# Kernel optimization log

Measured on AMD Instinct MI355X. Metric: run time of the kernel, lower is better.

Reference implementation:

```python
import jax, jax.numpy as jnp
import numpy as np

B, R, H, IN, L = 8, 128, 256, 512, 3
NH, DH = 4, H // 4  # attention heads


def _layernorm(x, g, b, eps=1e-5):
    mu = jnp.mean(x, axis=-1, keepdims=True)
    var = jnp.mean(jnp.square(x - mu), axis=-1, keepdims=True)
    return (x - mu) * jax.lax.rsqrt(var + eps) * g + b


def setup_inputs() -> dict:
    key = jax.random.key(0)
    ks = iter(jax.random.split(key, 40))
    s = 0.02
    d = {}
    d['x'] = jax.random.normal(next(ks), (B, IN), jnp.float32)
    d['We'] = jax.random.normal(next(ks), (IN, H), jnp.float32) * s
    d['be'] = jnp.zeros((H,), jnp.float32)
    # per-graph-layer params, stacked along leading L axis
    d['msg_W1'] = jax.random.normal(next(ks), (L, 2 * H, H), jnp.float32) * s
    d['msg_b1'] = jnp.zeros((L, H), jnp.float32)
    d['msg_W2'] = jax.random.normal(next(ks), (L, H, H), jnp.float32) * s
    d['msg_b2'] = jnp.zeros((L, H), jnp.float32)
    d['upd_W1'] = jax.random.normal(next(ks), (L, 2 * H, H), jnp.float32) * s
    d['upd_b1'] = jnp.zeros((L, H), jnp.float32)
    d['upd_W2'] = jax.random.normal(next(ks), (L, H, H), jnp.float32) * s
    d['upd_b2'] = jnp.zeros((L, H), jnp.float32)
    d['ln_g'] = jnp.ones((L, H), jnp.float32)
    d['ln_b'] = jnp.zeros((L, H), jnp.float32)
    d['rule_adj'] = jax.random.normal(next(ks), (R, R), jnp.float32)
    # multihead attention (4 heads)
    d['Wq'] = jax.random.normal(next(ks), (H, H), jnp.float32) * s
    d['bq'] = jnp.zeros((H,), jnp.float32)
    d['Wk'] = jax.random.normal(next(ks), (H, H), jnp.float32) * s
    d['bk'] = jnp.zeros((H,), jnp.float32)
    d['Wv'] = jax.random.normal(next(ks), (H, H), jnp.float32) * s
    d['bv'] = jnp.zeros((H,), jnp.float32)
    d['Wo'] = jax.random.normal(next(ks), (H, H), jnp.float32) * s
    d['bo'] = jnp.zeros((H,), jnp.float32)
    # readout MLP -> num_rules logits
    d['ro_W1'] = jax.random.normal(next(ks), (H, H), jnp.float32) * s
    d['ro_b1'] = jnp.zeros((H,), jnp.float32)
    d['ro_W2'] = jax.random.normal(next(ks), (H, R), jnp.float32) * s
    d['ro_b2'] = jnp.zeros((R,), jnp.float32)
    return d


def reference(x, We, be, msg_W1, msg_b1, msg_W2, msg_b2,
              upd_W1, upd_b1, upd_W2, upd_b2, ln_g, ln_b, rule_adj,
              Wq, bq, Wk, bk, Wv, bv, Wo, bo,
              ro_W1, ro_b1, ro_W2, ro_b2):
    # node encoder, broadcast to all rule-graph nodes: [B,R,H]
    h0 = x @ We + be
    h = jnp.broadcast_to(h0[:, None, :], (B, R, H))
    # rule adjacency with self-edges excluded (loop used i != j)
    A = jax.nn.sigmoid(rule_adj) * (1.0 - jnp.eye(R, dtype=rule_adj.dtype))  # [R,R]
    for l in range(L):
        # message_net(cat(h_i, h_j)) = relu(h_i@W1a + h_j@W1b + b1)@W2 + b2
        W1a, W1b = msg_W1[l][:H], msg_W1[l][H:]
        a = h @ W1a   # [B,R,H] (receiver i part)
        bb = h @ W1b  # [B,R,H] (sender j part)
        pre = jax.nn.relu(a[:, :, None, :] + bb[:, None, :, :] + msg_b1[l])  # [B,R,R,H]
        m = pre @ msg_W2[l] + msg_b2[l]  # [B,R,R,H] message from j to i
        agg = jnp.einsum('bijh,ij->bih', m, A)  # weighted sum over senders j
        # update_net(cat(h, agg))
        Wu1a, Wu1b = upd_W1[l][:H], upd_W1[l][H:]
        u = jax.nn.relu(h @ Wu1a + agg @ Wu1b + upd_b1[l]) @ upd_W2[l] + upd_b2[l]
        h = _layernorm(h + u, ln_g[l], ln_b[l])
    # multihead self-attention over nodes
    q = (h @ Wq + bq).reshape(B, R, NH, DH)
    k = (h @ Wk + bk).reshape(B, R, NH, DH)
    v = (h @ Wv + bv).reshape(B, R, NH, DH)
    logits = jnp.einsum('bqhd,bkhd->bhqk', q, k) / jnp.sqrt(jnp.float32(DH))
    attn = jax.nn.softmax(logits, axis=-1)
    pooled = jnp.einsum('bhqk,bkhd->bqhd', attn, v).reshape(B, R, H) @ Wo + bo
    g = jnp.mean(pooled, axis=1)  # [B,H]
    rule_logits = jax.nn.relu(g @ ro_W1 + ro_b1) @ ro_W2 + ro_b2
    rule_probabilities = jax.nn.softmax(rule_logits, axis=-1)  # [B,R]
    return rule_probabilities
```

## Files before the change

### kernel.cpp

```cpp
#include <hip/hip_runtime.h>
#include <math.h>

constexpr int NB  = 8;
constexpr int NR  = 128;
constexpr int HID = 256;
constexpr int NIN = 512;
constexpr int DHD = 64;
constexpr size_t SZ = (size_t)NB * NR * HID;

struct KP {
    const float *x, *We, *be, *msg_W1, *msg_b1, *msg_W2, *msg_b2;
    const float *upd_W1, *upd_b1, *upd_W2, *upd_b2, *ln_g, *ln_b, *rule_adj;
    const float *Wq, *bq, *Wk, *bk, *Wv, *bv, *Wo, *bo, *ro_W1, *ro_b1, *ro_W2, *ro_b2;
    float* out;
    float *N0, *N1, *N2;
    float *aB, *bbB, *p1B;
    float *aA, *bbA, *p1A;
    float *W2u, *mb2u, *Aw, *rsum;
    float *mW1s;
    float *h0g, *c0g, *c1g;
    float *gacc;
    float *scratch;
};

__device__ __forceinline__ void gemm_core(
    float (&As)[16][68], float (&Bs)[16][64], int m0, int n0,
    const float* __restrict__ A, const float* __restrict__ B,
    float (&acc)[4][4])
{
    int tid = threadIdx.x;
    int ty = tid >> 4, tx = tid & 15;
    int arow = tid >> 2, acol = (tid & 3) << 2;
    int brow = tid >> 4, bcol = (tid & 15) << 2;
    int m = m0 + arow;

    float4 av = *(const float4*)&A[(size_t)m * HID + acol];
    float4 bv = *(const float4*)&B[(size_t)brow * HID + n0 + bcol];

    for (int k0 = 0; k0 < HID; k0 += 16) {
        As[acol + 0][arow] = av.x;
        As[acol + 1][arow] = av.y;
        As[acol + 2][arow] = av.z;
        As[acol + 3][arow] = av.w;
        *(float4*)&Bs[brow][bcol] = bv;
        __syncthreads();
        if (k0 + 16 < HID) {
            av = *(const float4*)&A[(size_t)m * HID + k0 + 16 + acol];
            bv = *(const float4*)&B[(size_t)(k0 + 16 + brow) * HID + n0 + bcol];
        }
#pragma unroll
        for (int kk = 0; kk < 16; ++kk) {
            float4 af = *(const float4*)&As[kk][ty << 2];
            float4 bf = *(const float4*)&Bs[kk][tx << 2];
            float a_[4] = {af.x, af.y, af.z, af.w};
            float b_[4] = {bf.x, bf.y, bf.z, bf.w};
#pragma unroll
            for (int i = 0; i < 4; ++i)
#pragma unroll
                for (int j = 0; j < 4; ++j) acc[i][j] += a_[i] * b_[j];
        }
        __syncthreads();
    }
}

__device__ __forceinline__ void gemv256w(
    const float* xs, const float* __restrict__ W,
    const float* __restrict__ bias, int relu, float* ys, float* red)
{
    int tid = threadIdx.x;
    int w = tid >> 6, l = tid & 63;
    float4 acc = {0.f, 0.f, 0.f, 0.f};
    const float* Wp = W + (size_t)(w * 64) * HID + l * 4;
    const float* xp = xs + w * 64;
#pragma unroll 16
    for (int kk = 0; kk < 64; ++kk) {
        float xv = xp[kk];
        float4 wv = *(const float4*)(Wp + (size_t)kk * HID);
        acc.x += xv * wv.x; acc.y += xv * wv.y;
        acc.z += xv * wv.z; acc.w += xv * wv.w;
    }
    *(float4*)&red[w * 256 + l * 4] = acc;
    __syncthreads();
    float v = red[tid] + red[256 + tid] + red[512 + tid] + red[768 + tid];
    if (bias) v += bias[tid];
    if (relu) v = fmaxf(v, 0.0f);
    ys[tid] = v;
    __syncthreads();
}

__device__ __forceinline__ void rows4_half(
    const float (&rows)[4][HID], const float* __restrict__ W,
    int col, int half, float o[4])
{
    o[0] = o[1] = o[2] = o[3] = 0.f;
    int kbase = half * 128;
#pragma unroll 4
    for (int k0 = 0; k0 < 128; k0 += 4) {
        int k = kbase + k0;
        float w0 = W[(size_t)(k + 0) * HID + col];
        float w1 = W[(size_t)(k + 1) * HID + col];
        float w2 = W[(size_t)(k + 2) * HID + col];
        float w3 = W[(size_t)(k + 3) * HID + col];
#pragma unroll
        for (int ii = 0; ii < 4; ++ii) {
            float4 rv = *(const float4*)&rows[ii][k];
            o[ii] += rv.x * w0 + rv.y * w1 + rv.z * w2 + rv.w * w3;
        }
    }
}

__device__ __forceinline__ void ln_stats4_512(
    float (&sred)[4][4][2], float (&mi)[4][2], const float v[4], int half)
{
    if (half == 0) {
        int w = threadIdx.x >> 6, l = threadIdx.x & 63;
        float s[4], q[4];
#pragma unroll
        for (int ii = 0; ii < 4; ++ii) { s[ii] = v[ii]; q[ii] = v[ii] * v[ii]; }
#pragma unroll
        for (int off = 32; off; off >>= 1) {
#pragma unroll
            for (int ii = 0; ii < 4; ++ii) {
                s[ii] += __shfl_xor(s[ii], off);
                q[ii] += __shfl_xor(q[ii], off);
            }
        }
        if (l == 0) {
#pragma unroll
            for (int ii = 0; ii < 4; ++ii) { sred[w][ii][0] = s[ii]; sred[w][ii][1] = q[ii]; }
        }
    }
    __syncthreads();
    if (threadIdx.x < 4) {
        int r = threadIdx.x;
        float ss = sred[0][r][0] + sred[1][r][0] + sred[2][r][0] + sred[3][r][0];
        float qq = sred[0][r][1] + sred[1][r][1] + sred[2][r][1] + sred[3][r][1];
        float mu = ss * (1.0f / HID);
        mi[r][0] = mu;
        mi[r][1] = rsqrtf(qq * (1.0f / HID) - mu * mu + 1e-5f);
    }
    __syncthreads();
}

__global__ __launch_bounds__(256) void setup0_kernel(KP P) {
    __shared__ union {
        struct { float As[16][68]; float Bs[16][64]; } g;
        struct { float xs[NIN]; float part[8][32]; } e;
    } L;
    int blk = blockIdx.x;
    int t = threadIdx.x;

    if (blk < 32) {
        int rr = blk * 4 + (t >> 6);
        int l = t & 63;
        float s_loc = 0.f;
#pragma unroll
        for (int rep = 0; rep < 2; ++rep) {
            int j = l + rep * 64;
            float xv = P.rule_adj[rr * NR + j];
            float sg = 1.0f / (1.0f + expf(-xv));
            if (j == rr) sg = 0.0f;
            P.Aw[rr * NR + j] = sg;
            s_loc += sg;
        }
#pragma unroll
        for (int off = 32; off; off >>= 1) s_loc += __shfl_xor(s_loc, off);
        if (l == 0) P.rsum[rr] = s_loc;
    } else if (blk < 80) {
        int idx = blk - 32, l2 = idx >> 4, t16 = idx & 15;
        int m0 = (t16 >> 2) * 64, n0 = (t16 & 3) * 64;
        float acc[4][4] = {};
        gemm_core(L.g.As, L.g.Bs, m0, n0,
                  P.msg_W2 + (size_t)l2 * HID * HID,
                  P.upd_W1 + (size_t)l2 * 2 * HID * HID + (size_t)HID * HID,
                  acc);
        int ty = t >> 4, tx = t & 15;
        float* C = P.W2u + (size_t)l2 * HID * HID;
#pragma unroll
        for (int i = 0; i < 4; ++i) {
            int m = m0 + (ty << 2) + i, n = n0 + (tx << 2);
            float4 o = {acc[i][0], acc[i][1], acc[i][2], acc[i][3]};
            *(float4*)&C[(size_t)m * HID + n] = o;
        }
    } else if (blk < 83) {
        int l2 = blk - 80;
        const float* b2v = P.msg_b2 + l2 * HID;
        const float* Bm = P.upd_W1 + (size_t)l2 * 2 * HID * HID + (size_t)HID * HID;
        float acc = 0.f;
#pragma unroll 4
        for (int k = 0; k < HID; ++k) acc += b2v[k] * Bm[(size_t)k * HID + t];
        P.mb2u[l2 * HID + t] = acc;
    } else if (blk < 147) {
        int idx = blk - 83;
        int b = idx >> 3, s = idx & 7;
        L.e.xs[t]       = P.x[b * NIN + t];
        L.e.xs[256 + t] = P.x[b * NIN + 256 + t];
        __syncthreads();
        int c = t & 31, seg = t >> 5;
        int col = s * 32 + c;
        const float* Wp = P.We + (size_t)(seg * 64) * HID + col;
        const float* xp = L.e.xs + seg * 64;
        float acc = 0.f;
#pragma unroll 16
        for (int k = 0; k < 64; ++k) acc += xp[k] * Wp[(size_t)k * HID];
        L.e.part[seg][c] = acc;
        __syncthreads();
        if (t < 32) {
            float v = 0.f;
#pragma unroll
            for (int sg = 0; sg < 8; ++sg) v += L.e.part[sg][t];
            int cc = s * 32 + t;
            P.h0g[b * HID + cc] = v + P.be[cc];
        }
    } else if (blk < 163) {
        int base = (blk - 147) * 4096;
        for (int i = t; i < 4096; i += 256) {
            int o = base + i;
            P.mW1s[o] = P.msg_W1[o] + P.msg_W1[65536 + o];
        }
    } else {
        int pfid = blk - 163, npf = 256 - 163;
        const float* arr[11] = {P.We, P.msg_W1, P.msg_W2, P.upd_W1, P.upd_W2,
                                P.Wq, P.Wk, P.Wv, P.Wo, P.ro_W1, P.ro_W2};
        const int n4[11] = {32768, 98304, 49152, 98304, 49152,
                            16384, 16384, 16384, 16384, 16384, 8192};
        float s = 0.f;
        for (int a = 0; a < 11; ++a) {
            const float4* p4 = (const float4*)arr[a];
            for (int i = pfid * 256 + t; i < n4[a]; i += npf * 256) {
                float4 v = p4[i];
                s += v.x + v.y + v.z + v.w;
            }
        }
        if (s == 1.0e37f) P.scratch[pfid] = s;
    }
}

__global__ __launch_bounds__(256) void headc_kernel(KP P) {
    __shared__ float h0s[HID];
    __shared__ float p0s[HID];
    __shared__ float part[8][32];
    int blk = blockIdx.x;
    int z = blk >> 6, bs = blk & 63;
    int b = bs >> 3, s = bs & 7;
    int t = threadIdx.x;
    h0s[t] = P.h0g[b * HID + t];
    __syncthreads();
    const float* Wslice;
    const float* xs;
    if (z == 0) {
        Wslice = P.upd_W1;
        xs = h0s;
    } else {
        float accp = 0.f;
#pragma unroll 8
        for (int k = 0; k < HID; ++k)
            accp += h0s[k] * P.mW1s[(size_t)k * HID + t];
        p0s[t] = fmaxf(accp + P.msg_b1[t], 0.0f);
        __syncthreads();
        Wslice = P.W2u;
        xs = p0s;
    }
    int c = t & 31, seg = t >> 5;
    int col = s * 32 + c;
    const float* Wp = Wslice + (size_t)(seg * 32) * HID + col;
    const float* xp = xs + seg * 32;
    float acc = 0.f;
#pragma unroll 8
    for (int k = 0; k < 32; ++k) acc += xp[k] * Wp[(size_t)k * HID];
    part[seg][c] = acc;
    __syncthreads();
    if (t < 32) {
        float v = 0.f;
#pragma unroll
        for (int sg = 0; sg < 8; ++sg) v += part[sg][t];
        int cc = s * 32 + t;
        if (z == 0) P.c0g[b * HID + cc] = v;
        else        P.c1g[b * HID + cc] = v + P.mb2u[cc];
    }
}

__global__ __launch_bounds__(512) void layer0p_kernel(KP P) {
    __shared__ float u1s[4][HID];
    __shared__ float nrm[4][HID];
    __shared__ float part[2][4][HID];
    __shared__ float sred[4][4][2];
    __shared__ float mi[4][2];
    int blk = blockIdx.x;
    int m0 = blk * 4;
    int b = m0 >> 7, i0 = m0 & 127;
    int t = threadIdx.x;
    int col = t & 255, half = t >> 8;

    if (half == 0) {
        float c0v = P.c0g[b * HID + col];
        float c1v = P.c1g[b * HID + col];
        float ubv = P.upd_b1[col];
#pragma unroll
        for (int ii = 0; ii < 4; ++ii)
            u1s[ii][col] = fmaxf(c0v + P.rsum[i0 + ii] * c1v + ubv, 0.0f);
    }
    __syncthreads();

    float o[4], u[4];
    rows4_half(u1s, P.upd_W2, col, half, o);
#pragma unroll
    for (int ii = 0; ii < 4; ++ii) part[half][ii][col] = o[ii];
    __syncthreads();
#pragma unroll
    for (int ii = 0; ii < 4; ++ii) u[ii] = part[0][ii][col] + part[1][ii][col];

    float v[4] = {0.f, 0.f, 0.f, 0.f};
    if (half == 0) {
        float h0v = P.h0g[b * HID + col] + P.upd_b2[col];
#pragma unroll
        for (int ii = 0; ii < 4; ++ii) v[ii] = u[ii] + h0v;
    }
    ln_stats4_512(sred, mi, v, half);
    if (half == 0) {
        float gv = P.ln_g[col], btv = P.ln_b[col];
#pragma unroll
        for (int ii = 0; ii < 4; ++ii) {
            float nv = (v[ii] - mi[ii][0]) * mi[ii][1] * gv + btv;
            nrm[ii][col] = nv;
            P.N0[(size_t)(m0 + ii) * HID + col] = nv;
        }
    }
    __syncthreads();

    const float* mW1a1 = P.msg_W1 + (size_t)1 * 2 * HID * HID;
    const float* uW1a1 = P.upd_W1 + (size_t)1 * 2 * HID * HID;
    const float* pw[3] = {mW1a1, mW1a1 + (size_t)HID * HID, uW1a1};
    float* po[3] = {P.aB, P.bbB, P.p1B};
#pragma unroll
    for (int p = 0; p < 3; ++p) {
        rows4_half(nrm, pw[p], col, half, o);
#pragma unroll
        for (int ii = 0; ii < 4; ++ii) part[half][ii][col] = o[ii];
        __syncthreads();
        if (half == 0) {
#pragma unroll
            for (int ii = 0; ii < 4; ++ii)
                po[p][(size_t)(m0 + ii) * HID + col] = part[0][ii][col] + part[1][ii][col];
        }
        __syncthreads();
    }
}

__global__ __launch_bounds__(512) void aggproj_kernel(
    const float* __restrict__ a, const float* __restrict__ bbv,
    const float* __restrict__ mb1, const float* __restrict__ Aw,
    const float* __restrict__ rsumv,
    const float* __restrict__ P1, const float* __restrict__ W2u,
    const float* __restrict__ mb2u, const float* __restrict__ ub1,
    const float* __restrict__ uW2, const float* __restrict__ ub2,
    const float* __restrict__ Nprev, const float* __restrict__ lng,
    const float* __restrict__ lnb, float* __restrict__ Nout,
    const float* __restrict__ pw0, const float* __restrict__ pb0, float* __restrict__ o0,
    const float* __restrict__ pw1, const float* __restrict__ pb1, float* __restrict__ o1,
    const float* __restrict__ pw2, const float* __restrict__ pb2, float* __restrict__ o2,
    float* __restrict__ gzero)
{
    __shared__ float ap[4][HID];
    __shared__ float u1s[4][HID];
    __shared__ float nrm[4][HID];
    __shared__ float awr[4][NR];
    __shared__ float part[2][4][HID];
    __shared__ float sred[4][4][2];
    __shared__ float mi[4][2];
    int blk = blockIdx.x;
    int b  = blk >> 5;
    int i0 = (blk & 31) * 4;
    int m0 = b * NR + i0;
    int t  = threadIdx.x;
    int col = t & 255, half = t >> 8;

    if (gzero && blk == 0 && half == 0) {
#pragma unroll
        for (int i = 0; i < 8; ++i) gzero[i * 256 + col] = 0.f;
    }

    awr[t >> 7][t & 127] = Aw[(i0 + (t >> 7)) * NR + (t & 127)];

    float bias = mb1[col];
    float ai[4];
#pragma unroll
    for (int ii = 0; ii < 4; ++ii)
        ai[ii] = a[(size_t)(m0 + ii) * HID + col] + bias;
    __syncthreads();

    {
        float acc[4] = {0.f, 0.f, 0.f, 0.f};
        const float* bbb = &bbv[(size_t)b * NR * HID + col];
        int jb = half * 64;
#pragma unroll 4
        for (int j = 0; j < 64; ++j) {
            float bj = bbb[(size_t)(jb + j) * HID];
#pragma unroll
            for (int ii = 0; ii < 4; ++ii) {
                float pre = fmaxf(ai[ii] + bj, 0.0f);
                acc[ii] += awr[ii][jb + j] * pre;
            }
        }
#pragma unroll
        for (int ii = 0; ii < 4; ++ii) part[half][ii][col] = acc[ii];
        __syncthreads();
        if (half == 0) {
#pragma unroll
            for (int ii = 0; ii < 4; ++ii)
                ap[ii][col] = part[0][ii][col] + part[1][ii][col];
        }
        __syncthreads();
    }

    {
        float o[4];
        rows4_half(ap, W2u, col, half, o);
#pragma unroll
        for (int ii = 0; ii < 4; ++ii) part[half][ii][col] = o[ii];
        __syncthreads();
        if (half == 0) {
            float mbv = mb2u[col], ubv = ub1[col];
#pragma unroll
            for (int ii = 0; ii < 4; ++ii) {
                float w2f = part[0][ii][col] + part[1][ii][col];
                float vv = w2f + P1[(size_t)(m0 + ii) * HID + col]
                         + rsumv[i0 + ii] * mbv + ubv;
                u1s[ii][col] = fmaxf(vv, 0.0f);
            }
        }
        __syncthreads();
    }

    {
        float o[4];
        rows4_half(u1s, uW2, col, half, o);
#pragma unroll
        for (int ii = 0; ii < 4; ++ii) part[half][ii][col] = o[ii];
        __syncthreads();
        float v[4] = {0.f, 0.f, 0.f, 0.f};
        if (half == 0) {
            float ub2v = ub2[col];
#pragma unroll
            for (int ii = 0; ii < 4; ++ii) {
                float uf = part[0][ii][col] + part[1][ii][col];
                v[ii] = Nprev[(size_t)(m0 + ii) * HID + col] + uf + ub2v;
            }
        }
        ln_stats4_512(sred, mi, v, half);
        if (half == 0) {
            float gv = lng[col], btv = lnb[col];
#pragma unroll
            for (int ii = 0; ii < 4; ++ii) {
                float nv = (v[ii] - mi[ii][0]) * mi[ii][1] * gv + btv;
                nrm[ii][col] = nv;
                Nout[(size_t)(m0 + ii) * HID + col] = nv;
            }
        }
        __syncthreads();
    }

    {
        const float* pw[3] = {pw0, pw1, pw2};
        const float* pb[3] = {pb0, pb1, pb2};
        float* po[3] = {o0, o1, o2};
#pragma unroll
        for (int p = 0; p < 3; ++p) {
            float o[4];
            rows4_half(nrm, pw[p], col, half, o);
#pragma unroll
            for (int ii = 0; ii < 4; ++ii) part[half][ii][col] = o[ii];
            __syncthreads();
            if (half == 0) {
                float pbv = pb[p] ? pb[p][col] : 0.f;
#pragma unroll
                for (int ii = 0; ii < 4; ++ii)
                    po[p][(size_t)(m0 + ii) * HID + col] =
                        part[0][ii][col] + part[1][ii][col] + pbv;
            }
            __syncthreads();
        }
    }
}

__global__ __launch_bounds__(256) void attention_kernel(
    const float* __restrict__ q, const float* __restrict__ k,
    const float* __restrict__ v, float* __restrict__ gacc)
{
    __shared__ struct { float KhT[64][128]; float S[16][128]; float qs[16][64]; } L;
    int blk = blockIdx.x;
    int bh = blk >> 3, ig = blk & 7;
    int b = bh >> 2, hd = bh & 3;
    int i0 = ig * 16;
    int t = threadIdx.x;
    const float* qg = q + ((size_t)b * NR) * HID + hd * DHD;
    const float* kg = k + ((size_t)b * NR) * HID + hd * DHD;
    const float* vg = v + ((size_t)b * NR) * HID + hd * DHD;

    {
        int j = t >> 1, half = t & 1;
        const float* krow = kg + (size_t)j * HID + half * 32;
#pragma unroll
        for (int c = 0; c < 32; c += 4) {
            float4 kv = *(const float4*)(krow + c);
            L.KhT[half * 32 + c + 0][j] = kv.x;
            L.KhT[half * 32 + c + 1][j] = kv.y;
            L.KhT[half * 32 + c + 2][j] = kv.z;
            L.KhT[half * 32 + c + 3][j] = kv.w;
        }
    }
    {
        int ii = t >> 4, d0 = (t & 15) * 4;
        *(float4*)&L.qs[ii][d0] = *(const float4*)(qg + (size_t)(i0 + ii) * HID + d0);
    }
    __syncthreads();
    {
        int j = t & 127, ii2 = t >> 7;
        float acc[8] = {0.f,0.f,0.f,0.f,0.f,0.f,0.f,0.f};
#pragma unroll 4
        for (int d = 0; d < 64; ++d) {
            float kv = L.KhT[d][j];
#pragma unroll
            for (int ii = 0; ii < 8; ++ii) acc[ii] += L.qs[ii2 * 8 + ii][d] * kv;
        }
#pragma unroll
        for (int ii = 0; ii < 8; ++ii) L.S[ii2 * 8 + ii][j] = acc[ii] * 0.125f;
    }
    __syncthreads();
    {
        int w = t >> 6, l = t & 63;
#pragma unroll
        for (int r = w * 4; r < w * 4 + 4; ++r) {
            float e0 = L.S[r][l], e1 = L.S[r][l + 64];
            float mx = fmaxf(e0, e1);
#pragma unroll
            for (int off = 32; off; off >>= 1) mx = fmaxf(mx, __shfl_xor(mx, off));
            e0 = expf(e0 - mx); e1 = expf(e1 - mx);
            float sm = e0 + e1;
#pragma unroll
            for (int off = 32; off; off >>= 1) sm += __shfl_xor(sm, off);
            float inv = 1.0f / sm;
            L.S[r][l] = e0 * inv; L.S[r][l + 64] = e1 * inv;
        }
    }
    __syncthreads();
    {
        int d = t & 63, ir = t >> 6;
        float accv[4] = {0.f, 0.f, 0.f, 0.f};
        const float* vp = vg + d;
#pragma unroll 8
        for (int j = 0; j < NR; ++j) {
            float vv = vp[(size_t)j * HID];
#pragma unroll
            for (int p = 0; p < 4; ++p) accv[p] += L.S[p * 4 + ir][j] * vv;
        }
        float s = accv[0] + accv[1] + accv[2] + accv[3];
        atomicAdd(&gacc[b * HID + hd * DHD + d], s);
    }
}

__global__ __launch_bounds__(256) void tailf_kernel(KP P) {
    __shared__ float v0[HID], v1[HID], v2[HID];
    __shared__ float red[1024];
    int b = blockIdx.x;
    int t = threadIdx.x;
    int w = t >> 6, l = t & 63;

    v0[t] = P.gacc[b * HID + t] * (1.0f / NR);
    __syncthreads();
    gemv256w(v0, P.Wo, P.bo, 0, v1, red);
    gemv256w(v1, P.ro_W1, P.ro_b1, 1, v2, red);

    {
        float2 acc = {0.f, 0.f};
        const float* Wp = P.ro_W2 + (size_t)(w * 64) * NR + l * 2;
        const float* xp = v2 + w * 64;
#pragma unroll 8
        for (int kk = 0; kk < 64; ++kk) {
            float xv = xp[kk];
            float2 wv = *(const float2*)(Wp + (size_t)kk * NR);
            acc.x += xv * wv.x; acc.y += xv * wv.y;
        }
        *(float2*)&red[w * 128 + l * 2] = acc;
        __syncthreads();
    }
    float logit = -1e30f;
    if (t < NR) logit = red[t] + red[128 + t] + red[256 + t] + red[384 + t] + P.ro_b2[t];
    __syncthreads();
    float m = logit;
#pragma unroll
    for (int off = 32; off; off >>= 1) m = fmaxf(m, __shfl_xor(m, off));
    if (l == 0) red[w] = m;
    __syncthreads();
    m = fmaxf(red[0], red[1]);
    float e = (t < NR) ? expf(logit - m) : 0.0f;
    float ssum = e;
#pragma unroll
    for (int off = 32; off; off >>= 1) ssum += __shfl_xor(ssum, off);
    if (l == 0) red[4 + w] = ssum;
    __syncthreads();
    float tot = red[4] + red[5];
    if (t < NR) P.out[b * NR + t] = e / tot;
}

extern "C" void kernel_launch(void* const* d_in, const int* in_sizes, int n_in,
                              void* d_out, int out_size, void* d_ws, size_t ws_size,
                              hipStream_t stream)
{
    KP P;
    P.x        = (const float*)d_in[0];
    P.We       = (const float*)d_in[1];
    P.be       = (const float*)d_in[2];
    P.msg_W1   = (const float*)d_in[3];
    P.msg_b1   = (const float*)d_in[4];
    P.msg_W2   = (const float*)d_in[5];
    P.msg_b2   = (const float*)d_in[6];
    P.upd_W1   = (const float*)d_in[7];
    P.upd_b1   = (const float*)d_in[8];
    P.upd_W2   = (const float*)d_in[9];
    P.upd_b2   = (const float*)d_in[10];
    P.ln_g     = (const float*)d_in[11];
    P.ln_b     = (const float*)d_in[12];
    P.rule_adj = (const float*)d_in[13];
    P.Wq       = (const float*)d_in[14];
    P.bq       = (const float*)d_in[15];
    P.Wk       = (const float*)d_in[16];
    P.bk       = (const float*)d_in[17];
    P.Wv       = (const float*)d_in[18];
    P.bv       = (const float*)d_in[19];
    P.Wo       = (const float*)d_in[20];
    P.bo       = (const float*)d_in[21];
    P.ro_W1    = (const float*)d_in[22];
    P.ro_b1    = (const float*)d_in[23];
    P.ro_W2    = (const float*)d_in[24];
    P.ro_b2    = (const float*)d_in[25];
    P.out      = (float*)d_out;

    float* b0 = (float*)d_ws;
    P.N0     = b0;  b0 += SZ;
    P.N1     = b0;  b0 += SZ;
    P.N2     = b0;  b0 += SZ;
    P.aB     = b0;  b0 += SZ;
    P.bbB    = b0;  b0 += SZ;
    P.p1B    = b0;  b0 += SZ;
    P.aA     = b0;  b0 += SZ;
    P.bbA    = b0;  b0 += SZ;
    P.p1A    = b0;  b0 += SZ;
    P.W2u    = b0;  b0 += 3 * HID * HID;
    P.mb2u   = b0;  b0 += 3 * HID;
    P.mW1s   = b0;  b0 += HID * HID;
    P.Aw     = b0;  b0 += NR * NR;
    P.rsum   = b0;  b0 += NR;
    P.h0g    = b0;  b0 += NB * HID;
    P.c0g    = b0;  b0 += NB * HID;
    P.c1g    = b0;  b0 += NB * HID;
    P.gacc   = b0;  b0 += NB * HID;
    P.scratch= b0;  b0 += 256;

    setup0_kernel<<<dim3(256), 256, 0, stream>>>(P);

    headc_kernel<<<dim3(128), 256, 0, stream>>>(P);

    layer0p_kernel<<<dim3(256), 512, 0, stream>>>(P);

    {
        const int l = 1;
        const float* mW1a2 = P.msg_W1 + (size_t)2 * 2 * HID * HID;
        const float* uW1a2 = P.upd_W1 + (size_t)2 * 2 * HID * HID;
        aggproj_kernel<<<dim3(256), 512, 0, stream>>>(
            P.aB, P.bbB, P.msg_b1 + (size_t)l * HID, P.Aw, P.rsum,
            P.p1B, P.W2u + (size_t)l * HID * HID, P.mb2u + l * HID,
            P.upd_b1 + (size_t)l * HID,
            P.upd_W2 + (size_t)l * HID * HID, P.upd_b2 + (size_t)l * HID,
            P.N0, P.ln_g + (size_t)l * HID, P.ln_b + (size_t)l * HID, P.N1,
            mW1a2, nullptr, P.aA,
            mW1a2 + (size_t)HID * HID, nullptr, P.bbA,
            uW1a2, nullptr, P.p1A,
            nullptr);
    }

    {
        const int l = 2;
        aggproj_kernel<<<dim3(256), 512, 0, stream>>>(
            P.aA, P.bbA, P.msg_b1 + (size_t)l * HID, P.Aw, P.rsum,
            P.p1A, P.W2u + (size_t)l * HID * HID, P.mb2u + l * HID,
            P.upd_b1 + (size_t)l * HID,
            P.upd_W2 + (size_t)l * HID * HID, P.upd_b2 + (size_t)l * HID,
            P.N1, P.ln_g + (size_t)l * HID, P.ln_b + (size_t)l * HID, P.N2,
            P.Wq, P.bq, P.aB,
            P.Wk, P.bk, P.bbB,
            P.Wv, P.bv, P.p1B,
            P.gacc);
    }

    attention_kernel<<<dim3(256), 256, 0, stream>>>(P.aB, P.bbB, P.p1B, P.gacc);

    tailf_kernel<<<dim3(8), 256, 0, stream>>>(P);
}
```

Baseline: 258.6 us.

## Fold head-constant kernel into layer0 and split K four ways with 1024-thread blocks

Removes the separate headc kernel launch by recomputing the per-batch c0/c1 vectors inside each layer0p block through shared-memory GEMVs. Both layer0p and aggproj now use 1024 threads, splitting each reduction into four K-quarters instead of two. This cuts one launch and shortens each thread's serial reduction chain. In exchange, the c0/c1 GEMVs are repeated redundantly in all 256 blocks, the 4-way shared-memory reduction is larger, and occupancy may drop with 1024-thread blocks.

```diff
diff --git a/kernel.cpp b/kernel.cpp
--- a/kernel.cpp
+++ b/kernel.cpp
@@ -18,7 +18,7 @@
     float *aA, *bbA, *p1A;
     float *W2u, *mb2u, *Aw, *rsum;
     float *mW1s;
-    float *h0g, *c0g, *c1g;
+    float *h0g;
     float *gacc;
     float *scratch;
 };
@@ -88,15 +88,15 @@
     __syncthreads();
 }
 
-__device__ __forceinline__ void rows4_half(
+__device__ __forceinline__ void rows4_q(
     const float (&rows)[4][HID], const float* __restrict__ W,
-    int col, int half, float o[4])
+    int col, int q, float o[4])
 {
     o[0] = o[1] = o[2] = o[3] = 0.f;
-    int kbase = half * 128;
+    int kb = q * 64;
 #pragma unroll 4
-    for (int k0 = 0; k0 < 128; k0 += 4) {
-        int k = kbase + k0;
+    for (int k0 = 0; k0 < 64; k0 += 4) {
+        int k = kb + k0;
         float w0 = W[(size_t)(k + 0) * HID + col];
         float w1 = W[(size_t)(k + 1) * HID + col];
         float w2 = W[(size_t)(k + 2) * HID + col];
@@ -109,25 +109,36 @@
     }
 }
 
-__device__ __forceinline__ void ln_stats4_512(
-    float (&sred)[4][4][2], float (&mi)[4][2], const float v[4], int half)
-{
-    if (half == 0) {
+__device__ __forceinline__ float gemv_q(
+    const float* xs, const float* __restrict__ W, int col, int q)
+{
+    float o = 0.f;
+    int kb = q * 64;
+#pragma unroll 8
+    for (int k = 0; k < 64; ++k)
+        o += xs[kb + k] * W[(size_t)(kb + k) * HID + col];
+    return o;
+}
+
+__device__ __forceinline__ void ln_stats4_q(
+    float (&sred)[4][4][2], float (&mi)[4][2], const float v[4], int q)
+{
+    if (q == 0) {
         int w = threadIdx.x >> 6, l = threadIdx.x & 63;
-        float s[4], q[4];
-#pragma unroll
-        for (int ii = 0; ii < 4; ++ii) { s[ii] = v[ii]; q[ii] = v[ii] * v[ii]; }
+        float s[4], qq[4];
+#pragma unroll
+        for (int ii = 0; ii < 4; ++ii) { s[ii] = v[ii]; qq[ii] = v[ii] * v[ii]; }
 #pragma unroll
         for (int off = 32; off; off >>= 1) {
 #pragma unroll
             for (int ii = 0; ii < 4; ++ii) {
                 s[ii] += __shfl_xor(s[ii], off);
-                q[ii] += __shfl_xor(q[ii], off);
+                qq[ii] += __shfl_xor(qq[ii], off);
             }
         }
         if (l == 0) {
 #pragma unroll
-            for (int ii = 0; ii < 4; ++ii) { sred[w][ii][0] = s[ii]; sred[w][ii][1] = q[ii]; }
+            for (int ii = 0; ii < 4; ++ii) { sred[w][ii][0] = s[ii]; sred[w][ii][1] = qq[ii]; }
         }
     }
     __syncthreads();
@@ -236,88 +247,58 @@
     }
 }
 
-__global__ __launch_bounds__(256) void headc_kernel(KP P) {
-    __shared__ float h0s[HID];
-    __shared__ float p0s[HID];
-    __shared__ float part[8][32];
-    int blk = blockIdx.x;
-    int z = blk >> 6, bs = blk & 63;
-    int b = bs >> 3, s = bs & 7;
-    int t = threadIdx.x;
-    h0s[t] = P.h0g[b * HID + t];
-    __syncthreads();
-    const float* Wslice;
-    const float* xs;
-    if (z == 0) {
-        Wslice = P.upd_W1;
-        xs = h0s;
-    } else {
-        float accp = 0.f;
-#pragma unroll 8
-        for (int k = 0; k < HID; ++k)
-            accp += h0s[k] * P.mW1s[(size_t)k * HID + t];
-        p0s[t] = fmaxf(accp + P.msg_b1[t], 0.0f);
-        __syncthreads();
-        Wslice = P.W2u;
-        xs = p0s;
-    }
-    int c = t & 31, seg = t >> 5;
-    int col = s * 32 + c;
-    const float* Wp = Wslice + (size_t)(seg * 32) * HID + col;
-    const float* xp = xs + seg * 32;
-    float acc = 0.f;
-#pragma unroll 8
-    for (int k = 0; k < 32; ++k) acc += xp[k] * Wp[(size_t)k * HID];
-    part[seg][c] = acc;
-    __syncthreads();
-    if (t < 32) {
-        float v = 0.f;
-#pragma unroll
-        for (int sg = 0; sg < 8; ++sg) v += part[sg][t];
-        int cc = s * 32 + t;
-        if (z == 0) P.c0g[b * HID + cc] = v;
-        else        P.c1g[b * HID + cc] = v + P.mb2u[cc];
-    }
-}
-
-__global__ __launch_bounds__(512) void layer0p_kernel(KP P) {
+__global__ __launch_bounds__(1024) void layer0p_kernel(KP P) {
+    __shared__ float h0s[HID], p0s[HID], c0s[HID], c1s[HID];
     __shared__ float u1s[4][HID];
     __shared__ float nrm[4][HID];
-    __shared__ float part[2][4][HID];
+    __shared__ float part4[4][4][HID];
     __shared__ float sred[4][4][2];
     __shared__ float mi[4][2];
     int blk = blockIdx.x;
     int m0 = blk * 4;
     int b = m0 >> 7, i0 = m0 & 127;
     int t = threadIdx.x;
-    int col = t & 255, half = t >> 8;
-
-    if (half == 0) {
-        float c0v = P.c0g[b * HID + col];
-        float c1v = P.c1g[b * HID + col];
+    int col = t & 255, q = t >> 8;
+
+    if (q == 0) h0s[col] = P.h0g[b * HID + col];
+    __syncthreads();
+
+    part4[q][0][col] = gemv_q(h0s, P.upd_W1, col, q);
+    part4[q][1][col] = gemv_q(h0s, P.mW1s, col, q);
+    __syncthreads();
+    if (q == 0) {
+        c0s[col] = part4[0][0][col] + part4[1][0][col] + part4[2][0][col] + part4[3][0][col];
+        float pv = part4[0][1][col] + part4[1][1][col] + part4[2][1][col] + part4[3][1][col];
+        p0s[col] = fmaxf(pv + P.msg_b1[col], 0.0f);
+    }
+    __syncthreads();
+    part4[q][0][col] = gemv_q(p0s, P.W2u, col, q);
+    __syncthreads();
+    if (q == 0) {
+        c1s[col] = part4[0][0][col] + part4[1][0][col] + part4[2][0][col] + part4[3][0][col]
+                 + P.mb2u[col];
         float ubv = P.upd_b1[col];
 #pragma unroll
         for (int ii = 0; ii < 4; ++ii)
-            u1s[ii][col] = fmaxf(c0v + P.rsum[i0 + ii] * c1v + ubv, 0.0f);
-    }
-    __syncthreads();
-
-    float o[4], u[4];
-    rows4_half(u1s, P.upd_W2, col, half, o);
-#pragma unroll
-    for (int ii = 0; ii < 4; ++ii) part[half][ii][col] = o[ii];
-    __syncthreads();
-#pragma unroll
-    for (int ii = 0; ii < 4; ++ii) u[ii] = part[0][ii][col] + part[1][ii][col];
-
+            u1s[ii][col] = fmaxf(c0s[col] + P.rsum[i0 + ii] * c1s[col] + ubv, 0.0f);
+    }
+    __syncthreads();
+
+    float o[4];
+    rows4_q(u1s, P.upd_W2, col, q, o);
+#pragma unroll
+    for (int ii = 0; ii < 4; ++ii) part4[q][ii][col] = o[ii];
+    __syncthreads();
     float v[4] = {0.f, 0.f, 0.f, 0.f};
-    if (half == 0) {
-        float h0v = P.h0g[b * HID + col] + P.upd_b2[col];
-#pragma unroll
-        for (int ii = 0; ii < 4; ++ii) v[ii] = u[ii] + h0v;
-    }
-    ln_stats4_512(sred, mi, v, half);
-    if (half == 0) {
+    if (q == 0) {
+        float h0v = h0s[col] + P.upd_b2[col];
+#pragma unroll
+        for (int ii = 0; ii < 4; ++ii)
+            v[ii] = part4[0][ii][col] + part4[1][ii][col] + part4[2][ii][col]
+                  + part4[3][ii][col] + h0v;
+    }
+    ln_stats4_q(sred, mi, v, q);
+    if (q == 0) {
         float gv = P.ln_g[col], btv = P.ln_b[col];
 #pragma unroll
         for (int ii = 0; ii < 4; ++ii) {
@@ -334,20 +315,22 @@
     float* po[3] = {P.aB, P.bbB, P.p1B};
 #pragma unroll
     for (int p = 0; p < 3; ++p) {
-        rows4_half(nrm, pw[p], col, half, o);
-#pragma unroll
-        for (int ii = 0; ii < 4; ++ii) part[half][ii][col] = o[ii];
-        __syncthreads();
-        if (half == 0) {
+        rows4_q(nrm, pw[p], col, q, o);
+#pragma unroll
+        for (int ii = 0; ii < 4; ++ii) part4[q][ii][col] = o[ii];
+        __syncthreads();
+        if (q == 0) {
 #pragma unroll
             for (int ii = 0; ii < 4; ++ii)
-                po[p][(size_t)(m0 + ii) * HID + col] = part[0][ii][col] + part[1][ii][col];
-        }
-        __syncthreads();
-    }
-}
-
-__global__ __launch_bounds__(512) void aggproj_kernel(
+                po[p][(size_t)(m0 + ii) * HID + col] =
+                    part4[0][ii][col] + part4[1][ii][col] +
+                    part4[2][ii][col] + part4[3][ii][col];
+        }
+        __syncthreads();
+    }
+}
+
+__global__ __launch_bounds__(1024) void aggproj_kernel(
     const float* __restrict__ a, const float* __restrict__ bbv,
     const float* __restrict__ mb1, const float* __restrict__ Aw,
     const float* __restrict__ rsumv,
@@ -365,7 +348,7 @@
     __shared__ float u1s[4][HID];
     __shared__ float nrm[4][HID];
     __shared__ float awr[4][NR];
-    __shared__ float part[2][4][HID];
+    __shared__ float part4[4][4][HID];
     __shared__ float sred[4][4][2];
     __shared__ float mi[4][2];
     int blk = blockIdx.x;
@@ -373,14 +356,14 @@
     int i0 = (blk & 31) * 4;
     int m0 = b * NR + i0;
     int t  = threadIdx.x;
-    int col = t & 255, half = t >> 8;
-
-    if (gzero && blk == 0 && half == 0) {
+    int col = t & 255, q = t >> 8;
+
+    if (gzero && blk == 0 && q == 0) {
 #pragma unroll
         for (int i = 0; i < 8; ++i) gzero[i * 256 + col] = 0.f;
     }
 
-    awr[t >> 7][t & 127] = Aw[(i0 + (t >> 7)) * NR + (t & 127)];
+    if (t < 512) awr[t >> 7][t & 127] = Aw[(i0 + (t >> 7)) * NR + (t & 127)];
 
     float bias = mb1[col];
     float ai[4];
@@ -392,9 +375,9 @@
     {
         float acc[4] = {0.f, 0.f, 0.f, 0.f};
         const float* bbb = &bbv[(size_t)b * NR * HID + col];
-        int jb = half * 64;
+        int jb = q * 32;
 #pragma unroll 4
-        for (int j = 0; j < 64; ++j) {
+        for (int j = 0; j < 32; ++j) {
             float bj = bbb[(size_t)(jb + j) * HID];
 #pragma unroll
             for (int ii = 0; ii < 4; ++ii) {
@@ -403,27 +386,29 @@
             }
         }
 #pragma unroll
-        for (int ii = 0; ii < 4; ++ii) part[half][ii][col] = acc[ii];
-        __syncthreads();
-        if (half == 0) {
+        for (int ii = 0; ii < 4; ++ii) part4[q][ii][col] = acc[ii];
+        __syncthreads();
+        if (q == 0) {
 #pragma unroll
             for (int ii = 0; ii < 4; ++ii)
-                ap[ii][col] = part[0][ii][col] + part[1][ii][col];
+                ap[ii][col] = part4[0][ii][col] + part4[1][ii][col]
+                            + part4[2][ii][col] + part4[3][ii][col];
         }
         __syncthreads();
     }
 
     {
         float o[4];
-        rows4_half(ap, W2u, col, half, o);
-#pragma unroll
-        for (int ii = 0; ii < 4; ++ii) part[half][ii][col] = o[ii];
-        __syncthreads();
-        if (half == 0) {
+        rows4_q(ap, W2u, col, q, o);
+#pragma unroll
+        for (int ii = 0; ii < 4; ++ii) part4[q][ii][col] = o[ii];
+        __syncthreads();
+        if (q == 0) {
             float mbv = mb2u[col], ubv = ub1[col];
 #pragma unroll
             for (int ii = 0; ii < 4; ++ii) {
-                float w2f = part[0][ii][col] + part[1][ii][col];
+                float w2f = part4[0][ii][col] + part4[1][ii][col]
+                          + part4[2][ii][col] + part4[3][ii][col];
                 float vv = w2f + P1[(size_t)(m0 + ii) * HID + col]
                          + rsumv[i0 + ii] * mbv + ubv;
                 u1s[ii][col] = fmaxf(vv, 0.0f);
@@ -434,21 +419,22 @@
 
     {
         float o[4];
-        rows4_half(u1s, uW2, col, half, o);
-#pragma unroll
-        for (int ii = 0; ii < 4; ++ii) part[half][ii][col] = o[ii];
+        rows4_q(u1s, uW2, col, q, o);
+#pragma unroll
+        for (int ii = 0; ii < 4; ++ii) part4[q][ii][col] = o[ii];
         __syncthreads();
         float v[4] = {0.f, 0.f, 0.f, 0.f};
-        if (half == 0) {
+        if (q == 0) {
             float ub2v = ub2[col];
 #pragma unroll
             for (int ii = 0; ii < 4; ++ii) {
-                float uf = part[0][ii][col] + part[1][ii][col];
+                float uf = part4[0][ii][col] + part4[1][ii][col]
+                         + part4[2][ii][col] + part4[3][ii][col];
                 v[ii] = Nprev[(size_t)(m0 + ii) * HID + col] + uf + ub2v;
             }
         }
-        ln_stats4_512(sred, mi, v, half);
-        if (half == 0) {
+        ln_stats4_q(sred, mi, v, q);
+        if (q == 0) {
             float gv = lng[col], btv = lnb[col];
 #pragma unroll
             for (int ii = 0; ii < 4; ++ii) {
@@ -467,16 +453,17 @@
 #pragma unroll
         for (int p = 0; p < 3; ++p) {
             float o[4];
-            rows4_half(nrm, pw[p], col, half, o);
-#pragma unroll
-            for (int ii = 0; ii < 4; ++ii) part[half][ii][col] = o[ii];
+            rows4_q(nrm, pw[p], col, q, o);
+#pragma unroll
+            for (int ii = 0; ii < 4; ++ii) part4[q][ii][col] = o[ii];
             __syncthreads();
-            if (half == 0) {
+            if (q == 0) {
                 float pbv = pb[p] ? pb[p][col] : 0.f;
 #pragma unroll
                 for (int ii = 0; ii < 4; ++ii)
                     po[p][(size_t)(m0 + ii) * HID + col] =
-                        part[0][ii][col] + part[1][ii][col] + pbv;
+                        part4[0][ii][col] + part4[1][ii][col] +
+                        part4[2][ii][col] + part4[3][ii][col] + pbv;
             }
             __syncthreads();
         }
@@ -652,22 +639,18 @@
     P.Aw     = b0;  b0 += NR * NR;
     P.rsum   = b0;  b0 += NR;
     P.h0g    = b0;  b0 += NB * HID;
-    P.c0g    = b0;  b0 += NB * HID;
-    P.c1g    = b0;  b0 += NB * HID;
     P.gacc   = b0;  b0 += NB * HID;
     P.scratch= b0;  b0 += 256;
 
     setup0_kernel<<<dim3(256), 256, 0, stream>>>(P);
 
-    headc_kernel<<<dim3(128), 256, 0, stream>>>(P);
-
-    layer0p_kernel<<<dim3(256), 512, 0, stream>>>(P);
+    layer0p_kernel<<<dim3(256), 1024, 0, stream>>>(P);
 
     {
         const int l = 1;
         const float* mW1a2 = P.msg_W1 + (size_t)2 * 2 * HID * HID;
         const float* uW1a2 = P.upd_W1 + (size_t)2 * 2 * HID * HID;
-        aggproj_kernel<<<dim3(256), 512, 0, stream>>>(
+        aggproj_kernel<<<dim3(256), 1024, 0, stream>>>(
             P.aB, P.bbB, P.msg_b1 + (size_t)l * HID, P.Aw, P.rsum,
             P.p1B, P.W2u + (size_t)l * HID * HID, P.mb2u + l * HID,
             P.upd_b1 + (size_t)l * HID,
@@ -681,7 +664,7 @@
 
     {
         const int l = 2;
-        aggproj_kernel<<<dim3(256), 512, 0, stream>>>(
+        aggproj_kernel<<<dim3(256), 1024, 0, stream>>>(
             P.aA, P.bbA, P.msg_b1 + (size_t)l * HID, P.Aw, P.rsum,
             P.p1A, P.W2u + (size_t)l * HID * HID, P.mb2u + l * HID,
             P.upd_b1 + (size_t)l * HID,
```

New measurement: 231.8 us, median of 2. 1.12x faster.
